# Kernel optimization log

Hardware: AMD Instinct MI355X
Metric: run time of the kernel (lower is better)

The kernel has to match this reference:

```python
import jax, jax.numpy as jnp
import numpy as np

N_NODES = 10000
NEG_SLOPE_ATT = 0.5   # GATConv negative_slope
NEG_SLOPE_ACT = 0.01  # F.leaky_relu default used as self.act


def setup_inputs() -> dict:
    key = jax.random.key(0)
    k1, k2, k3, k4, k5 = jax.random.split(key, 5)
    in_dim, out_dim = 512, 128
    x = jax.random.normal(k1, (N_NODES, in_dim), dtype=jnp.float32)
    edge_index = jax.random.randint(k2, (2, 320000), 0, N_NODES, dtype=jnp.int64)
    # glorot-ish scaled params
    W = jax.random.normal(k3, (in_dim, out_dim), dtype=jnp.float32) * (1.0 / np.sqrt(in_dim))
    att_src = jax.random.normal(k4, (out_dim,), dtype=jnp.float32) * (1.0 / np.sqrt(out_dim))
    att_dst = jax.random.normal(k5, (out_dim,), dtype=jnp.float32) * (1.0 / np.sqrt(out_dim))
    bias = jnp.zeros((out_dim,), dtype=jnp.float32)
    return {"x": x, "edge_index": edge_index, "W": W,
            "att_src": att_src, "att_dst": att_dst, "bias": bias}


def _leaky(v, slope):
    return jnp.where(v >= 0, v, slope * v)


def reference(x, edge_index, W, att_src, att_dst, bias):
    N = x.shape[0]
    loop = jnp.arange(N, dtype=edge_index.dtype)
    src = jnp.concatenate([edge_index[0], loop])  # message source j
    dst = jnp.concatenate([edge_index[1], loop])  # message target i

    h = x @ W                      # [N, out_dim]
    a_src = h @ att_src            # [N]
    a_dst = h @ att_dst            # [N]

    e = _leaky(a_src[src] + a_dst[dst], NEG_SLOPE_ATT)   # [E+N]
    # segment softmax over incoming edges of each dst node
    m = jax.ops.segment_max(e, dst, num_segments=N)
    ex = jnp.exp(e - m[dst])
    denom = jax.ops.segment_sum(ex, dst, num_segments=N)
    alpha = ex / denom[dst]

    out = jax.ops.segment_sum(h[src] * alpha[:, None], dst, num_segments=N) + bias
    embed_x = _leaky(out, NEG_SLOPE_ACT)                 # self.act = F.leaky_relu
    recon = jax.nn.sigmoid(embed_x @ embed_x.T)          # [N, N]
    return recon, embed_x
```

## Files before the change

### kernel.cpp

```cpp
#include <hip/hip_runtime.h>
#include <stdint.h>


typedef __attribute__((ext_vector_type(8))) short short8v;
typedef __attribute__((ext_vector_type(4))) float f32x4;

#define IN_DIM 512
#define OUT_DIM 128
#define NEG_ATT 0.5f
#define NEG_ACT 0.01f

__device__ __forceinline__ float leakyf(float v, float s) { return v >= 0.f ? v : s * v; }

__device__ __forceinline__ uint16_t f2bf(float v) {
  uint32_t u = __float_as_uint(v);
  u += 0x7FFFu + ((u >> 16) & 1u);
  return (uint16_t)(u >> 16);
}

__global__ __launch_bounds__(256) void k_h_gemm(const float* __restrict__ x,
                                                const float* __restrict__ W,
                                                const float* __restrict__ att_s_g,
                                                const float* __restrict__ att_d_g,
                                                const int* __restrict__ e_dst,
                                                int* __restrict__ cnt, int E,
                                                float* __restrict__ h,
                                                float* __restrict__ a_src,
                                                float* __restrict__ a_dst, int N) {
  int tid = threadIdx.x;
  int tx = tid & 31, ty = tid >> 5;
  int row0 = blockIdx.x * 16 + ty * 2;
  int rc[2];
  #pragma unroll
  for (int r = 0; r < 2; ++r) rc[r] = (row0 + r < N) ? (row0 + r) : (N - 1);

  f32x4 acc[2];
  #pragma unroll
  for (int r = 0; r < 2; ++r) acc[r] = (f32x4){0.f, 0.f, 0.f, 0.f};

  for (int k = 0; k < IN_DIM; k += 4) {
    f32x4 wreg[4];
    #pragma unroll
    for (int kk = 0; kk < 4; ++kk)
      wreg[kk] = *(const f32x4*)&W[(size_t)(k + kk) * OUT_DIM + tx * 4];
    #pragma unroll
    for (int r = 0; r < 2; ++r) {
      f32x4 xv = *(const f32x4*)&x[(size_t)rc[r] * IN_DIM + k];
      #pragma unroll
      for (int kk = 0; kk < 4; ++kk) {
        acc[r][0] = fmaf(xv[kk], wreg[kk][0], acc[r][0]);
        acc[r][1] = fmaf(xv[kk], wreg[kk][1], acc[r][1]);
        acc[r][2] = fmaf(xv[kk], wreg[kk][2], acc[r][2]);
        acc[r][3] = fmaf(xv[kk], wreg[kk][3], acc[r][3]);
      }
    }
  }

  float atts[4], attd[4];
  #pragma unroll
  for (int j = 0; j < 4; ++j) { atts[j] = att_s_g[tx * 4 + j]; attd[j] = att_d_g[tx * 4 + j]; }
  #pragma unroll
  for (int r = 0; r < 2; ++r) {
    int row = row0 + r;
    float ps = 0.f, pd = 0.f;
    #pragma unroll
    for (int j = 0; j < 4; ++j) { ps = fmaf(acc[r][j], atts[j], ps); pd = fmaf(acc[r][j], attd[j], pd); }
    #pragma unroll
    for (int off = 16; off; off >>= 1) {
      ps += __shfl_xor(ps, off);
      pd += __shfl_xor(pd, off);
    }
    if (row < N) {
      *(f32x4*)&h[(size_t)row * OUT_DIM + tx * 4] = acc[r];
      if (tx == 0) { a_src[row] = ps; a_dst[row] = pd; }
    }
  }

  int e0 = blockIdx.x * 512 + tid;
  if (e0 < E) atomicAdd(&cnt[e_dst[e0]], 1);
  int e1 = e0 + 256;
  if (e1 < E) atomicAdd(&cnt[e_dst[e1]], 1);
}

__global__ __launch_bounds__(1024) void k_scan(const int* __restrict__ cnt,
                                               int* __restrict__ row_start,
                                               int* __restrict__ cursor, int N) {
  __shared__ int sd[1024];
  int t = threadIdx.x;
  const int CH = (N + 1023) >> 10;
  int base = t * CH;
  int s = 0;
  for (int k = 0; k < CH; ++k) { int i = base + k; if (i < N) s += cnt[i]; }
  sd[t] = s;
  __syncthreads();
  for (int off = 1; off < 1024; off <<= 1) {
    int v = (t >= off) ? sd[t - off] : 0;
    __syncthreads();
    sd[t] += v;
    __syncthreads();
  }
  int run = (t == 0) ? 0 : sd[t - 1];
  for (int k = 0; k < CH; ++k) {
    int i = base + k;
    if (i < N) { row_start[i] = run; cursor[i] = run; run += cnt[i]; }
  }
  if (t == 1023) row_start[N] = sd[1023];
}
__global__ void k_fill(const int* __restrict__ src, const int* __restrict__ dst,
                       int* __restrict__ cursor, int* __restrict__ csr, int E) {
  int e = blockIdx.x * blockDim.x + threadIdx.x;
  if (e < E) {
    int d = dst[e];
    int pos = atomicAdd(&cursor[d], 1);
    csr[pos] = src[e];
  }
}

__global__ __launch_bounds__(256) void k_aggregate(
    const float* __restrict__ h, const float* __restrict__ a_src,
    const float* __restrict__ a_dst, const int* __restrict__ row_start,
    const int* __restrict__ csr, const float* __restrict__ bias,
    float* __restrict__ embed_out, uint16_t* __restrict__ ebf, int N, int NPAD) {
  int wid = (int)((blockIdx.x * blockDim.x + threadIdx.x) >> 6);
  int lane = threadIdx.x & 63;
  if (wid >= N) {
    if (wid < NPAD) {
      ebf[(size_t)wid * OUT_DIM + lane] = 0;
      ebf[(size_t)wid * OUT_DIM + 64 + lane] = 0;
    }
    return;
  }
  int i = wid;
  int s0 = row_start[i], s1 = row_start[i + 1];
  float adst = a_dst[i];
  float eself = leakyf(a_src[i] + adst, NEG_ATT);
  float m = eself;
  for (int k = s0 + lane; k < s1; k += 64) {
    float e = leakyf(a_src[csr[k]] + adst, NEG_ATT);
    m = fmaxf(m, e);
  }
  #pragma unroll
  for (int off = 32; off; off >>= 1) m = fmaxf(m, __shfl_xor(m, off));
  float dsum = 0.f;
  for (int k = s0 + lane; k < s1; k += 64) {
    float e = leakyf(a_src[csr[k]] + adst, NEG_ATT);
    dsum += __expf(e - m);
  }
  #pragma unroll
  for (int off = 32; off; off >>= 1) dsum += __shfl_xor(dsum, off);
  dsum += __expf(eself - m);
  float inv = 1.0f / dsum;
  float wself = __expf(eself - m) * inv;
  float acc0 = h[(size_t)i * OUT_DIM + lane] * wself;
  float acc1 = h[(size_t)i * OUT_DIM + 64 + lane] * wself;
  #pragma unroll 4
  for (int k = s0; k < s1; ++k) {
    int s = csr[k];
    float w = __expf(leakyf(a_src[s] + adst, NEG_ATT) - m) * inv;
    acc0 = fmaf(h[(size_t)s * OUT_DIM + lane], w, acc0);
    acc1 = fmaf(h[(size_t)s * OUT_DIM + 64 + lane], w, acc1);
  }
  float o0 = leakyf(acc0 + bias[lane], NEG_ACT);
  float o1 = leakyf(acc1 + bias[64 + lane], NEG_ACT);
  embed_out[(size_t)i * OUT_DIM + lane] = o0;
  embed_out[(size_t)i * OUT_DIM + 64 + lane] = o1;
  ebf[(size_t)i * OUT_DIM + lane] = f2bf(o0);
  ebf[(size_t)i * OUT_DIM + 64 + lane] = f2bf(o1);
}

__global__ __launch_bounds__(512, 4) void k_recon(const uint16_t* __restrict__ ebf,
                                                  float* __restrict__ out,
                                                  int N, int nb) {
  __shared__ __align__(16) unsigned char smem[66560];
  uint16_t* sA = (uint16_t*)smem;
  uint16_t* sB = (uint16_t*)(smem + 32768);
  float* sO = (float*)smem;

  int tid = threadIdx.x;
  int wid = tid >> 6, lane = tid & 63;
  int wr = wid >> 2, wc = wid & 3;
  int r16 = lane & 15, kg = lane >> 4;

  int nwg = nb * nb;
  int q = nwg >> 3, r8 = nwg & 7;
  int orig = blockIdx.x;
  int xcd = orig & 7, sub = orig >> 3;
  int swz = (xcd < r8 ? xcd * (q + 1) : r8 * (q + 1) + (xcd - r8) * q) + sub;
  int by = swz / nb, bx = swz - by * nb;
  int rowBlk = by * 128, colBlk = bx * 128;

  #pragma unroll
  for (int p = 0; p < 4; ++p) {
    int i2 = p * 512 + tid;
    int row = i2 >> 4, slot = i2 & 15;
    f32x4 va = *(const f32x4*)&ebf[(size_t)(rowBlk + row) * OUT_DIM + slot * 8];
    f32x4 vb = *(const f32x4*)&ebf[(size_t)(colBlk + row) * OUT_DIM + slot * 8];
    int ss = slot ^ (row & 7);
    *(f32x4*)&sA[row * OUT_DIM + ss * 8] = va;
    *(f32x4*)&sB[row * OUT_DIM + ss * 8] = vb;
  }
  __syncthreads();

  int rowWl = wr * 64, colWl = wc * 32;
  f32x4 acc[4][2];
  #pragma unroll
  for (int a = 0; a < 4; ++a)
    #pragma unroll
    for (int b = 0; b < 2; ++b) acc[a][b] = (f32x4){0.f, 0.f, 0.f, 0.f};

  #pragma unroll
  for (int kc = 0; kc < 4; ++kc) {
    short8v bfr[2];
    #pragma unroll
    for (int tj = 0; tj < 2; ++tj) {
      int rw = colWl + tj * 16 + r16;
      int ss = (kc * 4 + kg) ^ (rw & 7);
      bfr[tj] = *(const short8v*)&sB[rw * OUT_DIM + ss * 8];
    }
    #pragma unroll
    for (int ti = 0; ti < 4; ++ti) {
      int rw = rowWl + ti * 16 + r16;
      int ss = (kc * 4 + kg) ^ (rw & 7);
      short8v af = *(const short8v*)&sA[rw * OUT_DIM + ss * 8];
      #pragma unroll
      for (int tj = 0; tj < 2; ++tj)
        acc[ti][tj] = __builtin_amdgcn_mfma_f32_16x16x32_bf16(af, bfr[tj], acc[ti][tj], 0, 0, 0);
    }
  }

  bool colFull = (colBlk + 128 <= N);
  #pragma unroll
  for (int s = 0; s < 2; ++s) {
    __syncthreads();
    if (wr == s) {
      #pragma unroll
      for (int ti = 0; ti < 4; ++ti)
        #pragma unroll
        for (int tj = 0; tj < 2; ++tj)
          #pragma unroll
          for (int qq = 0; qq < 4; ++qq)
            sO[(ti * 16 + kg * 4 + qq) * 133 + wc * 32 + tj * 16 + r16] = acc[ti][tj][qq];
    }
    __syncthreads();
    int srow0 = rowBlk + s * 64;
    #pragma unroll
    for (int p = 0; p < 4; ++p) {
      int i2 = p * 512 + tid;
      int row = i2 >> 5, c = i2 & 31;
      f32x4 v = *(const f32x4*)&sO[row * 133 + c * 4];
      #pragma unroll
      for (int j = 0; j < 4; ++j) v[j] = 1.0f / (1.0f + __expf(-v[j]));
      int rr = srow0 + row;
      if (rr < N) {
        int col = colBlk + c * 4;
        if (colFull) {
          __builtin_nontemporal_store(v, (f32x4*)&out[(size_t)rr * N + col]);
        } else {
          #pragma unroll
          for (int j = 0; j < 4; ++j)
            if (col + j < N) __builtin_nontemporal_store(v[j], &out[(size_t)rr * N + col + j]);
        }
      }
    }
  }
}

extern "C" void kernel_launch(void* const* d_in, const int* in_sizes, int n_in,
                              void* d_out, int out_size, void* d_ws, size_t ws_size,
                              hipStream_t stream) {
  const float* x = (const float*)d_in[0];
  const int* ei = (const int*)d_in[1];
  const float* W = (const float*)d_in[2];
  const float* att_s = (const float*)d_in[3];
  const float* att_d = (const float*)d_in[4];
  const float* bias = (const float*)d_in[5];

  const int N = in_sizes[0] / IN_DIM;
  const int E = in_sizes[1] / 2;
  const int NB = (N + 127) / 128;
  const int NPAD = NB * 128;

  float* out = (float*)d_out;
  float* embed_out = out + (size_t)N * N;

  float* h = (float*)d_ws;
  float* a_src = h + (size_t)N * OUT_DIM;
  float* a_dst = a_src + N;
  int* cnt = (int*)(a_dst + N);
  int* row_start = cnt + N;
  int* cursor = row_start + (N + 4);
  int* csr = cursor + N;
  uint16_t* ebf = (uint16_t*)(csr + E);

  const int* e_src = ei;
  const int* e_dst = ei + E;

  hipMemsetAsync(cnt, 0, (size_t)N * sizeof(int), stream);
  k_h_gemm<<<dim3((N + 15) / 16), 256, 0, stream>>>(x, W, att_s, att_d,
                                                    e_dst, cnt, E, h, a_src, a_dst, N);
  k_scan<<<dim3(1), 1024, 0, stream>>>(cnt, row_start, cursor, N);
  k_fill<<<dim3((E + 255) / 256), 256, 0, stream>>>(e_src, e_dst, cursor, csr, E);
  k_aggregate<<<dim3((NPAD * 64 + 255) / 256), 256, 0, stream>>>(
      h, a_src, a_dst, row_start, csr, bias, embed_out, ebf, N, NPAD);
  k_recon<<<dim3(NB * NB), 512, 0, stream>>>(ebf, out, N, NB);
}
```

Measured before the change: 232.6 us.

## Store h in bf16 and shrink recon LDS footprint for higher occupancy

The projected features h are now stored as packed bf16, which halves the gather traffic in the aggregation kernel. The recon kernel stages B in two K-halves of 64 columns, cutting LDS use from 66.5KB to 48KB. The output staging is rewritten with an XOR swizzle in place of the 133 padding, and the occupancy hint is raised to 6. The cost is lower precision for h in the aggregation, plus extra barriers between the two K-halves in recon.

```diff
diff --git a/kernel.cpp b/kernel.cpp
--- a/kernel.cpp
+++ b/kernel.cpp
@@ -17,6 +17,7 @@
   u += 0x7FFFu + ((u >> 16) & 1u);
   return (uint16_t)(u >> 16);
 }
+__device__ __forceinline__ float bf2f(uint16_t b) { return __uint_as_float(((uint32_t)b) << 16); }
 
 __global__ __launch_bounds__(256) void k_h_gemm(const float* __restrict__ x,
                                                 const float* __restrict__ W,
@@ -24,7 +25,7 @@
                                                 const float* __restrict__ att_d_g,
                                                 const int* __restrict__ e_dst,
                                                 int* __restrict__ cnt, int E,
-                                                float* __restrict__ h,
+                                                uint16_t* __restrict__ h16,
                                                 float* __restrict__ a_src,
                                                 float* __restrict__ a_dst, int N) {
   int tid = threadIdx.x;
@@ -71,7 +72,10 @@
       pd += __shfl_xor(pd, off);
     }
     if (row < N) {
-      *(f32x4*)&h[(size_t)row * OUT_DIM + tx * 4] = acc[r];
+      uint32_t lo = (uint32_t)f2bf(acc[r][0]) | ((uint32_t)f2bf(acc[r][1]) << 16);
+      uint32_t hi = (uint32_t)f2bf(acc[r][2]) | ((uint32_t)f2bf(acc[r][3]) << 16);
+      uint2 pk; pk.x = lo; pk.y = hi;
+      *(uint2*)&h16[(size_t)row * OUT_DIM + tx * 4] = pk;
       if (tx == 0) { a_src[row] = ps; a_dst[row] = pd; }
     }
   }
@@ -117,7 +121,7 @@
 }
 
 __global__ __launch_bounds__(256) void k_aggregate(
-    const float* __restrict__ h, const float* __restrict__ a_src,
+    const uint16_t* __restrict__ h16, const float* __restrict__ a_src,
     const float* __restrict__ a_dst, const int* __restrict__ row_start,
     const int* __restrict__ csr, const float* __restrict__ bias,
     float* __restrict__ embed_out, uint16_t* __restrict__ ebf, int N, int NPAD) {
@@ -151,14 +155,14 @@
   dsum += __expf(eself - m);
   float inv = 1.0f / dsum;
   float wself = __expf(eself - m) * inv;
-  float acc0 = h[(size_t)i * OUT_DIM + lane] * wself;
-  float acc1 = h[(size_t)i * OUT_DIM + 64 + lane] * wself;
+  float acc0 = bf2f(h16[(size_t)i * OUT_DIM + lane]) * wself;
+  float acc1 = bf2f(h16[(size_t)i * OUT_DIM + 64 + lane]) * wself;
   #pragma unroll 4
   for (int k = s0; k < s1; ++k) {
     int s = csr[k];
     float w = __expf(leakyf(a_src[s] + adst, NEG_ATT) - m) * inv;
-    acc0 = fmaf(h[(size_t)s * OUT_DIM + lane], w, acc0);
-    acc1 = fmaf(h[(size_t)s * OUT_DIM + 64 + lane], w, acc1);
+    acc0 = fmaf(bf2f(h16[(size_t)s * OUT_DIM + lane]), w, acc0);
+    acc1 = fmaf(bf2f(h16[(size_t)s * OUT_DIM + 64 + lane]), w, acc1);
   }
   float o0 = leakyf(acc0 + bias[lane], NEG_ACT);
   float o1 = leakyf(acc1 + bias[64 + lane], NEG_ACT);
@@ -168,10 +172,10 @@
   ebf[(size_t)i * OUT_DIM + 64 + lane] = f2bf(o1);
 }
 
-__global__ __launch_bounds__(512, 4) void k_recon(const uint16_t* __restrict__ ebf,
+__global__ __launch_bounds__(512, 6) void k_recon(const uint16_t* __restrict__ ebf,
                                                   float* __restrict__ out,
                                                   int N, int nb) {
-  __shared__ __align__(16) unsigned char smem[66560];
+  __shared__ __align__(16) unsigned char smem[49152];
   uint16_t* sA = (uint16_t*)smem;
   uint16_t* sB = (uint16_t*)(smem + 32768);
   float* sO = (float*)smem;
@@ -194,10 +198,16 @@
     int i2 = p * 512 + tid;
     int row = i2 >> 4, slot = i2 & 15;
     f32x4 va = *(const f32x4*)&ebf[(size_t)(rowBlk + row) * OUT_DIM + slot * 8];
+    int ss = slot ^ (row & 7);
+    *(f32x4*)&sA[row * OUT_DIM + ss * 8] = va;
+  }
+  #pragma unroll
+  for (int p = 0; p < 2; ++p) {
+    int i2 = p * 512 + tid;
+    int row = i2 >> 3, slot = i2 & 7;
     f32x4 vb = *(const f32x4*)&ebf[(size_t)(colBlk + row) * OUT_DIM + slot * 8];
     int ss = slot ^ (row & 7);
-    *(f32x4*)&sA[row * OUT_DIM + ss * 8] = va;
-    *(f32x4*)&sB[row * OUT_DIM + ss * 8] = vb;
+    *(f32x4*)&sB[row * 64 + ss * 8] = vb;
   }
   __syncthreads();
 
@@ -209,37 +219,58 @@
     for (int b = 0; b < 2; ++b) acc[a][b] = (f32x4){0.f, 0.f, 0.f, 0.f};
 
   #pragma unroll
-  for (int kc = 0; kc < 4; ++kc) {
-    short8v bfr[2];
-    #pragma unroll
-    for (int tj = 0; tj < 2; ++tj) {
-      int rw = colWl + tj * 16 + r16;
-      int ss = (kc * 4 + kg) ^ (rw & 7);
-      bfr[tj] = *(const short8v*)&sB[rw * OUT_DIM + ss * 8];
-    }
-    #pragma unroll
-    for (int ti = 0; ti < 4; ++ti) {
-      int rw = rowWl + ti * 16 + r16;
-      int ss = (kc * 4 + kg) ^ (rw & 7);
-      short8v af = *(const short8v*)&sA[rw * OUT_DIM + ss * 8];
-      #pragma unroll
-      for (int tj = 0; tj < 2; ++tj)
-        acc[ti][tj] = __builtin_amdgcn_mfma_f32_16x16x32_bf16(af, bfr[tj], acc[ti][tj], 0, 0, 0);
-    }
-  }
+  for (int half = 0; half < 2; ++half) {
+    #pragma unroll
+    for (int kch = 0; kch < 2; ++kch) {
+      int s16 = (half * 2 + kch) * 4 + kg;
+      int khalf = kch * 4 + kg;
+      short8v bfr[2];
+      #pragma unroll
+      for (int tj = 0; tj < 2; ++tj) {
+        int rw = colWl + tj * 16 + r16;
+        int ss = khalf ^ (rw & 7);
+        bfr[tj] = *(const short8v*)&sB[rw * 64 + ss * 8];
+      }
+      #pragma unroll
+      for (int ti = 0; ti < 4; ++ti) {
+        int rw = rowWl + ti * 16 + r16;
+        int ss = s16 ^ (rw & 7);
+        short8v af = *(const short8v*)&sA[rw * OUT_DIM + ss * 8];
+        #pragma unroll
+        for (int tj = 0; tj < 2; ++tj)
+          acc[ti][tj] = __builtin_amdgcn_mfma_f32_16x16x32_bf16(af, bfr[tj], acc[ti][tj], 0, 0, 0);
+      }
+    }
+    if (half == 0) {
+      __syncthreads();
+      #pragma unroll
+      for (int p = 0; p < 2; ++p) {
+        int i2 = p * 512 + tid;
+        int row = i2 >> 3, slot = i2 & 7;
+        f32x4 vb = *(const f32x4*)&ebf[(size_t)(colBlk + row) * OUT_DIM + 64 + slot * 8];
+        int ss = slot ^ (row & 7);
+        *(f32x4*)&sB[row * 64 + ss * 8] = vb;
+      }
+      __syncthreads();
+    }
+  }
+  __syncthreads();
 
   bool colFull = (colBlk + 128 <= N);
   #pragma unroll
   for (int s = 0; s < 2; ++s) {
-    __syncthreads();
     if (wr == s) {
       #pragma unroll
       for (int ti = 0; ti < 4; ++ti)
         #pragma unroll
-        for (int tj = 0; tj < 2; ++tj)
+        for (int tj = 0; tj < 2; ++tj) {
+          int col = wc * 32 + tj * 16 + r16;
+          int slot = col >> 2, within = col & 3;
+          int sslot = slot ^ (kg << 1);
           #pragma unroll
           for (int qq = 0; qq < 4; ++qq)
-            sO[(ti * 16 + kg * 4 + qq) * 133 + wc * 32 + tj * 16 + r16] = acc[ti][tj][qq];
+            sO[(ti * 16 + kg * 4 + qq) * 128 + sslot * 4 + within] = acc[ti][tj][qq];
+        }
     }
     __syncthreads();
     int srow0 = rowBlk + s * 64;
@@ -247,7 +278,8 @@
     for (int p = 0; p < 4; ++p) {
       int i2 = p * 512 + tid;
       int row = i2 >> 5, c = i2 & 31;
-      f32x4 v = *(const f32x4*)&sO[row * 133 + c * 4];
+      int sslot = c ^ (((row >> 2) & 3) << 1);
+      f32x4 v = *(const f32x4*)&sO[row * 128 + sslot * 4];
       #pragma unroll
       for (int j = 0; j < 4; ++j) v[j] = 1.0f / (1.0f + __expf(-v[j]));
       int rr = srow0 + row;
@@ -262,6 +294,7 @@
         }
       }
     }
+    if (s == 0) __syncthreads();
   }
 }
 
@@ -283,8 +316,8 @@
   float* out = (float*)d_out;
   float* embed_out = out + (size_t)N * N;
 
-  float* h = (float*)d_ws;
-  float* a_src = h + (size_t)N * OUT_DIM;
+  uint16_t* h16 = (uint16_t*)d_ws;
+  float* a_src = (float*)(h16 + (size_t)N * OUT_DIM);
   float* a_dst = a_src + N;
   int* cnt = (int*)(a_dst + N);
   int* row_start = cnt + N;
@@ -297,10 +330,10 @@
 
   hipMemsetAsync(cnt, 0, (size_t)N * sizeof(int), stream);
   k_h_gemm<<<dim3((N + 15) / 16), 256, 0, stream>>>(x, W, att_s, att_d,
-                                                    e_dst, cnt, E, h, a_src, a_dst, N);
+                                                    e_dst, cnt, E, h16, a_src, a_dst, N);
   k_scan<<<dim3(1), 1024, 0, stream>>>(cnt, row_start, cursor, N);
   k_fill<<<dim3((E + 255) / 256), 256, 0, stream>>>(e_src, e_dst, cursor, csr, E);
   k_aggregate<<<dim3((NPAD * 64 + 255) / 256), 256, 0, stream>>>(
-      h, a_src, a_dst, row_start, csr, bias, embed_out, ebf, N, NPAD);
+      h16, a_src, a_dst, row_start, csr, bias, embed_out, ebf, N, NPAD);
   k_recon<<<dim3(NB * NB), 512, 0, stream>>>(ebf, out, N, NB);
 }
```

Result: faster. 225.1 us (median of 2 runs) (-3.3%).

## Exploit symmetry of recon matrix and store h in bf16

Applied to the files above, without the earlier changes.

The reconstruction kernel now launches only upper-triangular 128x128 tiles and writes each off-diagonal tile twice, once directly and once transposed through an XOR-swizzled shared-memory buffer. This roughly halves the MFMA work and the ebf loads. The output write volume, which likely dominates, is unchanged. Separately, h is stored as bf16 to halve the gather traffic in aggregation, which adds rounding error to embed_x.

```diff
diff --git a/kernel.cpp b/kernel.cpp
--- a/kernel.cpp
+++ b/kernel.cpp
@@ -1,5 +1,6 @@
 #include <hip/hip_runtime.h>
 #include <stdint.h>
+#include <math.h>
 
 
 typedef __attribute__((ext_vector_type(8))) short short8v;
@@ -17,6 +18,7 @@
   u += 0x7FFFu + ((u >> 16) & 1u);
   return (uint16_t)(u >> 16);
 }
+__device__ __forceinline__ float bf2f(uint16_t b) { return __uint_as_float(((uint32_t)b) << 16); }
 
 __global__ __launch_bounds__(256) void k_h_gemm(const float* __restrict__ x,
                                                 const float* __restrict__ W,
@@ -24,7 +26,7 @@
                                                 const float* __restrict__ att_d_g,
                                                 const int* __restrict__ e_dst,
                                                 int* __restrict__ cnt, int E,
-                                                float* __restrict__ h,
+                                                uint16_t* __restrict__ h16,
                                                 float* __restrict__ a_src,
                                                 float* __restrict__ a_dst, int N) {
   int tid = threadIdx.x;
@@ -71,7 +73,10 @@
       pd += __shfl_xor(pd, off);
     }
     if (row < N) {
-      *(f32x4*)&h[(size_t)row * OUT_DIM + tx * 4] = acc[r];
+      uint32_t lo = (uint32_t)f2bf(acc[r][0]) | ((uint32_t)f2bf(acc[r][1]) << 16);
+      uint32_t hi = (uint32_t)f2bf(acc[r][2]) | ((uint32_t)f2bf(acc[r][3]) << 16);
+      uint2 pk; pk.x = lo; pk.y = hi;
+      *(uint2*)&h16[(size_t)row * OUT_DIM + tx * 4] = pk;
       if (tx == 0) { a_src[row] = ps; a_dst[row] = pd; }
     }
   }
@@ -117,7 +122,7 @@
 }
 
 __global__ __launch_bounds__(256) void k_aggregate(
-    const float* __restrict__ h, const float* __restrict__ a_src,
+    const uint16_t* __restrict__ h16, const float* __restrict__ a_src,
     const float* __restrict__ a_dst, const int* __restrict__ row_start,
     const int* __restrict__ csr, const float* __restrict__ bias,
     float* __restrict__ embed_out, uint16_t* __restrict__ ebf, int N, int NPAD) {
@@ -151,14 +156,14 @@
   dsum += __expf(eself - m);
   float inv = 1.0f / dsum;
   float wself = __expf(eself - m) * inv;
-  float acc0 = h[(size_t)i * OUT_DIM + lane] * wself;
-  float acc1 = h[(size_t)i * OUT_DIM + 64 + lane] * wself;
+  float acc0 = bf2f(h16[(size_t)i * OUT_DIM + lane]) * wself;
+  float acc1 = bf2f(h16[(size_t)i * OUT_DIM + 64 + lane]) * wself;
   #pragma unroll 4
   for (int k = s0; k < s1; ++k) {
     int s = csr[k];
     float w = __expf(leakyf(a_src[s] + adst, NEG_ATT) - m) * inv;
-    acc0 = fmaf(h[(size_t)s * OUT_DIM + lane], w, acc0);
-    acc1 = fmaf(h[(size_t)s * OUT_DIM + 64 + lane], w, acc1);
+    acc0 = fmaf(bf2f(h16[(size_t)s * OUT_DIM + lane]), w, acc0);
+    acc1 = fmaf(bf2f(h16[(size_t)s * OUT_DIM + 64 + lane]), w, acc1);
   }
   float o0 = leakyf(acc0 + bias[lane], NEG_ACT);
   float o1 = leakyf(acc1 + bias[64 + lane], NEG_ACT);
@@ -171,7 +176,7 @@
 __global__ __launch_bounds__(512, 4) void k_recon(const uint16_t* __restrict__ ebf,
                                                   float* __restrict__ out,
                                                   int N, int nb) {
-  __shared__ __align__(16) unsigned char smem[66560];
+  __shared__ __align__(16) unsigned char smem[65536];
   uint16_t* sA = (uint16_t*)smem;
   uint16_t* sB = (uint16_t*)(smem + 32768);
   float* sO = (float*)smem;
@@ -181,12 +186,18 @@
   int wr = wid >> 2, wc = wid & 3;
   int r16 = lane & 15, kg = lane >> 4;
 
-  int nwg = nb * nb;
-  int q = nwg >> 3, r8 = nwg & 7;
+  int NT = nb * (nb + 1) / 2;
+  int q = NT >> 3, r8 = NT & 7;
   int orig = blockIdx.x;
   int xcd = orig & 7, sub = orig >> 3;
-  int swz = (xcd < r8 ? xcd * (q + 1) : r8 * (q + 1) + (xcd - r8) * q) + sub;
-  int by = swz / nb, bx = swz - by * nb;
+  int k = (xcd < r8 ? xcd * (q + 1) : r8 * (q + 1) + (xcd - r8) * q) + sub;
+  int by = (int)((2.0 * nb + 1.0 -
+                  sqrt((2.0 * nb + 1.0) * (2.0 * nb + 1.0) - 8.0 * (double)k)) * 0.5);
+  if (by < 0) by = 0;
+  if (by > nb - 1) by = nb - 1;
+  while ((by + 1) * nb - ((by + 1) * by) / 2 <= k) ++by;
+  while (by * nb - (by * (by - 1)) / 2 > k) --by;
+  int bx = by + (k - (by * nb - (by * (by - 1)) / 2));
   int rowBlk = by * 128, colBlk = bx * 128;
 
   #pragma unroll
@@ -227,39 +238,54 @@
         acc[ti][tj] = __builtin_amdgcn_mfma_f32_16x16x32_bf16(af, bfr[tj], acc[ti][tj], 0, 0, 0);
     }
   }
+  __syncthreads();
+
+  #pragma unroll
+  for (int ti = 0; ti < 4; ++ti)
+    #pragma unroll
+    for (int tj = 0; tj < 2; ++tj) {
+      int c = colWl + tj * 16 + r16;
+      #pragma unroll
+      for (int qq = 0; qq < 4; ++qq) {
+        int r = rowWl + ti * 16 + kg * 4 + qq;
+        float sg = 1.0f / (1.0f + __expf(-acc[ti][tj][qq]));
+        sO[r * 128 + (c ^ r)] = sg;
+      }
+    }
+  __syncthreads();
 
   bool colFull = (colBlk + 128 <= N);
   #pragma unroll
-  for (int s = 0; s < 2; ++s) {
-    __syncthreads();
-    if (wr == s) {
+  for (int p = 0; p < 8; ++p) {
+    int i2 = p * 512 + tid;
+    int row = i2 >> 5, cg = (i2 & 31) * 4;
+    int rr = rowBlk + row;
+    if (rr < N) {
+      f32x4 v;
       #pragma unroll
-      for (int ti = 0; ti < 4; ++ti)
+      for (int j = 0; j < 4; ++j) v[j] = sO[row * 128 + ((cg + j) ^ row)];
+      int col = colBlk + cg;
+      if (colFull) {
+        __builtin_nontemporal_store(v, (f32x4*)&out[(size_t)rr * N + col]);
+      } else {
         #pragma unroll
-        for (int tj = 0; tj < 2; ++tj)
-          #pragma unroll
-          for (int qq = 0; qq < 4; ++qq)
-            sO[(ti * 16 + kg * 4 + qq) * 133 + wc * 32 + tj * 16 + r16] = acc[ti][tj][qq];
-    }
-    __syncthreads();
-    int srow0 = rowBlk + s * 64;
-    #pragma unroll
-    for (int p = 0; p < 4; ++p) {
+        for (int j = 0; j < 4; ++j)
+          if (col + j < N) __builtin_nontemporal_store(v[j], &out[(size_t)rr * N + col + j]);
+      }
+    }
+  }
+
+  if (by != bx) {
+    #pragma unroll
+    for (int p = 0; p < 8; ++p) {
       int i2 = p * 512 + tid;
-      int row = i2 >> 5, c = i2 & 31;
-      f32x4 v = *(const f32x4*)&sO[row * 133 + c * 4];
-      #pragma unroll
-      for (int j = 0; j < 4; ++j) v[j] = 1.0f / (1.0f + __expf(-v[j]));
-      int rr = srow0 + row;
+      int u = i2 >> 5, cg = (i2 & 31) * 4;
+      int rr = colBlk + u;
       if (rr < N) {
-        int col = colBlk + c * 4;
-        if (colFull) {
-          __builtin_nontemporal_store(v, (f32x4*)&out[(size_t)rr * N + col]);
-        } else {
-          #pragma unroll
-          for (int j = 0; j < 4; ++j)
-            if (col + j < N) __builtin_nontemporal_store(v[j], &out[(size_t)rr * N + col + j]);
-        }
+        f32x4 v;
+        #pragma unroll
+        for (int j = 0; j < 4; ++j) v[j] = sO[(cg + j) * 128 + (u ^ (cg + j))];
+        __builtin_nontemporal_store(v, (f32x4*)&out[(size_t)rr * N + rowBlk + cg]);
       }
     }
   }
@@ -283,8 +309,8 @@
   float* out = (float*)d_out;
   float* embed_out = out + (size_t)N * N;
 
-  float* h = (float*)d_ws;
-  float* a_src = h + (size_t)N * OUT_DIM;
+  uint16_t* h16 = (uint16_t*)d_ws;
+  float* a_src = (float*)(h16 + (size_t)N * OUT_DIM);
   float* a_dst = a_src + N;
   int* cnt = (int*)(a_dst + N);
   int* row_start = cnt + N;
@@ -297,10 +323,11 @@
 
   hipMemsetAsync(cnt, 0, (size_t)N * sizeof(int), stream);
   k_h_gemm<<<dim3((N + 15) / 16), 256, 0, stream>>>(x, W, att_s, att_d,
-                                                    e_dst, cnt, E, h, a_src, a_dst, N);
+                                                    e_dst, cnt, E, h16, a_src, a_dst, N);
   k_scan<<<dim3(1), 1024, 0, stream>>>(cnt, row_start, cursor, N);
   k_fill<<<dim3((E + 255) / 256), 256, 0, stream>>>(e_src, e_dst, cursor, csr, E);
   k_aggregate<<<dim3((NPAD * 64 + 255) / 256), 256, 0, stream>>>(
-      h, a_src, a_dst, row_start, csr, bias, embed_out, ebf, N, NPAD);
-  k_recon<<<dim3(NB * NB), 512, 0, stream>>>(ebf, out, N, NB);
-}
+      h16, a_src, a_dst, row_start, csr, bias, embed_out, ebf, N, NPAD);
+  const int NT = NB * (NB + 1) / 2;
+  k_recon<<<dim3(NT), 512, 0, stream>>>(ebf, out, N, NB);
+}
```

New measurement: 230.0 us. Within noise of the previous version (-1.1%).
